# Kernel optimization log

Measured on AMD Instinct MI355X. Metric: run time of the kernel, lower is better.

## Reference

```python
import jax, jax.numpy as jnp
import numpy as np

D_MODEL = 1024
N_HEADS = 16
HEAD_DIM = D_MODEL // N_HEADS
B, S = 4, 2048
NEG = -1000000000.0


def setup_inputs() -> dict:
    key = jax.random.key(0)
    ks = jax.random.split(key, 13)
    sc = 1.0 / np.sqrt(D_MODEL)
    return {
        "query": jax.random.normal(ks[0], (B, S, D_MODEL), jnp.float32),
        "key": jax.random.normal(ks[1], (B, S, D_MODEL), jnp.float32),
        "value": jax.random.normal(ks[2], (B, S, D_MODEL), jnp.float32),
        "mask": jax.random.randint(ks[3], (B, 1, 1, S), 0, 2, jnp.int32),
        "Wq": jax.random.normal(ks[4], (D_MODEL, D_MODEL), jnp.float32) * sc,
        "bq": jax.random.normal(ks[5], (D_MODEL,), jnp.float32) * sc,
        "Wk": jax.random.normal(ks[6], (D_MODEL, D_MODEL), jnp.float32) * sc,
        "bk": jax.random.normal(ks[7], (D_MODEL,), jnp.float32) * sc,
        "Wv": jax.random.normal(ks[8], (D_MODEL, D_MODEL), jnp.float32) * sc,
        "bv": jax.random.normal(ks[9], (D_MODEL,), jnp.float32) * sc,
        "Wo": jax.random.normal(ks[10], (D_MODEL, D_MODEL), jnp.float32) * sc,
        "bo": jax.random.normal(ks[11], (D_MODEL,), jnp.float32) * sc,
    }


def _split_heads(x):
    b, s, _ = x.shape
    return x.reshape(b, s, N_HEADS, HEAD_DIM).transpose(0, 2, 1, 3)  # (B,H,S,Dh)


def reference(query, key, value, mask, Wq, bq, Wk, bk, Wv, bv, Wo, bo):
    # torch Linear: y = x @ W.T + b
    Q = _split_heads(query @ Wq.T + bq)
    K = _split_heads(key @ Wk.T + bk)
    V = _split_heads(value @ Wv.T + bv)
    scores = jnp.einsum("bhqd,bhkd->bhqk", Q, K) / np.sqrt(HEAD_DIM)
    scores = jnp.where(mask == 0, NEG, scores)
    probs = jax.nn.softmax(scores, axis=-1)
    ctx = jnp.einsum("bhqk,bhkd->bhqd", probs, V)
    ctx = ctx.transpose(0, 2, 1, 3).reshape(query.shape[0], query.shape[1], D_MODEL)
    return ctx @ Wo.T + bo
```

## Files before the change

kernel.cpp:

```cpp
#include <hip/hip_runtime.h>


typedef __bf16 bf16x8 __attribute__((ext_vector_type(8)));
typedef __bf16 bf16x4 __attribute__((ext_vector_type(4)));
typedef float  f32x4  __attribute__((ext_vector_type(4)));

#define LOG2E 1.44269504088896340736f
#define SCALE_Q (0.125f * LOG2E)
#define MBIAS_L2 (-1.44269504e9f)

__device__ inline unsigned short f2bf(float f) {
  unsigned int u = __float_as_uint(f);
  u = u + 0x7FFF + ((u >> 16) & 1);
  return (unsigned short)(u >> 16);
}
__device__ inline void gload16(const void* g, void* l) {
  __builtin_amdgcn_global_load_lds(
      (const __attribute__((address_space(1))) void*)g,
      (__attribute__((address_space(3))) void*)l, 16, 0, 0);
}
__device__ inline bf16x8 cvt8(const float* p) {
  float4 a = *(const float4*)p, b = *(const float4*)(p + 4);
  bf16x8 v;
  v[0] = (__bf16)a.x; v[1] = (__bf16)a.y; v[2] = (__bf16)a.z; v[3] = (__bf16)a.w;
  v[4] = (__bf16)b.x; v[5] = (__bf16)b.y; v[6] = (__bf16)b.z; v[7] = (__bf16)b.w;
  return v;
}

struct CvtJob { const float* s; unsigned short* d; int n8; };
struct CvtJobs { CvtJob j[7]; };
__global__ void cvt_all(CvtJobs J) {
  CvtJob jb = J.j[blockIdx.y];
  int i = blockIdx.x * 256 + threadIdx.x;
  if (i < jb.n8) *(bf16x8*)(jb.d + (size_t)i * 8) = cvt8(jb.s + (size_t)i * 8);
}

struct ProjJob { const unsigned short* A; const unsigned short* W;
                 const float* bias; unsigned short* out; float scale; };
struct ProjJobs { ProjJob j[3]; };

__global__ __launch_bounds__(256, 2) void gemm_qkv(ProjJobs J) {
  __shared__ __align__(16) unsigned short Al[128 * 32];
  __shared__ __align__(16) unsigned short Wl[128 * 32];
  const int z = blockIdx.z;
  const ProjJob jb = J.j[z];
  const int tid = threadIdx.x, lane = tid & 63, w = tid >> 6;
  const int lid = lane & 15, lg = lane >> 4;
  const int c0 = blockIdx.x * 128, t0 = blockIdx.y * 128;
  const int wm = (w & 1) * 64, wn = (w >> 1) * 64;
  const unsigned short* Ml = (z == 2) ? Al : Wl;
  const unsigned short* Nl = (z == 2) ? Wl : Al;

  f32x4 acc[4][4];
#pragma unroll
  for (int i = 0; i < 4; i++)
#pragma unroll
    for (int j = 0; j < 4; j++) acc[i][j] = (f32x4){0.f, 0.f, 0.f, 0.f};

  for (int kt = 0; kt < 1024; kt += 32) {
    __syncthreads();
#pragma unroll
    for (int i = 0; i < 2; i++) {
      int c = i * 256 + tid, r = c >> 2, ko = (c & 3) * 8;
      gload16(jb.A + (size_t)(t0 + r) * 1024 + kt + ko, &Al[c * 8]);
      gload16(jb.W + (size_t)(c0 + r) * 1024 + kt + ko, &Wl[c * 8]);
    }
    __syncthreads();
    bf16x8 mf[4], nf[4];
#pragma unroll
    for (int mi = 0; mi < 4; mi++)
      mf[mi] = *(const bf16x8*)(&Ml[(wm + mi * 16 + lid) * 32 + lg * 8]);
#pragma unroll
    for (int ni = 0; ni < 4; ni++)
      nf[ni] = *(const bf16x8*)(&Nl[(wn + ni * 16 + lid) * 32 + lg * 8]);
#pragma unroll
    for (int mi = 0; mi < 4; mi++)
#pragma unroll
      for (int ni = 0; ni < 4; ni++)
        acc[mi][ni] = __builtin_amdgcn_mfma_f32_16x16x32_bf16(mf[mi], nf[ni],
                                                              acc[mi][ni], 0, 0, 0);
  }

  if (z < 2) {
    const float scale = jb.scale;
#pragma unroll
    for (int mi = 0; mi < 4; mi++) {
      int colb = c0 + wm + mi * 16 + lg * 4;
      float4 b4 = *(const float4*)(&jb.bias[colb]);
#pragma unroll
      for (int ni = 0; ni < 4; ni++) {
        int token = t0 + wn + ni * 16 + lid;
        ushort4 st;
        st.x = f2bf((acc[mi][ni][0] + b4.x) * scale);
        st.y = f2bf((acc[mi][ni][1] + b4.y) * scale);
        st.z = f2bf((acc[mi][ni][2] + b4.z) * scale);
        st.w = f2bf((acc[mi][ni][3] + b4.w) * scale);
        *(ushort4*)(&jb.out[(size_t)token * 1024 + colb]) = st;
      }
    }
  } else {
    const int b = t0 >> 11;
#pragma unroll
    for (int ni = 0; ni < 4; ni++) {
      int col = c0 + wn + ni * 16 + lid;
      int h = col >> 6, d = col & 63;
      float bv = jb.bias[col];
#pragma unroll
      for (int mi = 0; mi < 4; mi++) {
        int s = (t0 & 2047) + wm + mi * 16 + lg * 4;
        ushort4 st;
        st.x = f2bf(acc[mi][ni][0] + bv);
        st.y = f2bf(acc[mi][ni][1] + bv);
        st.z = f2bf(acc[mi][ni][2] + bv);
        st.w = f2bf(acc[mi][ni][3] + bv);
        *(ushort4*)(&jb.out[(size_t)((b * 16 + h) * 64 + d) * 2048 + s]) = st;
      }
    }
  }
}

__global__ __launch_bounds__(256, 2) void gemm_o(
    const unsigned short* __restrict__ A, const unsigned short* __restrict__ W,
    const float* __restrict__ bias, float* __restrict__ C) {
  __shared__ __align__(16) unsigned short Al[128 * 32];
  __shared__ __align__(16) unsigned short Wl[128 * 32];
  const int tid = threadIdx.x, lane = tid & 63, w = tid >> 6;
  const int lid = lane & 15, lg = lane >> 4;
  const int c0 = blockIdx.x * 128, t0 = blockIdx.y * 128;
  const int wc = (w & 1) * 64, wt = (w >> 1) * 64;
  f32x4 acc[4][4];
#pragma unroll
  for (int i = 0; i < 4; i++)
#pragma unroll
    for (int j = 0; j < 4; j++) acc[i][j] = (f32x4){0.f, 0.f, 0.f, 0.f};

  for (int kt = 0; kt < 1024; kt += 32) {
    __syncthreads();
#pragma unroll
    for (int i = 0; i < 2; i++) {
      int c = i * 256 + tid, r = c >> 2, ko = (c & 3) * 8;
      gload16(A + (size_t)(t0 + r) * 1024 + kt + ko, &Al[c * 8]);
      gload16(W + (size_t)(c0 + r) * 1024 + kt + ko, &Wl[c * 8]);
    }
    __syncthreads();
    bf16x8 aw[4], bt[4];
#pragma unroll
    for (int mi = 0; mi < 4; mi++)
      aw[mi] = *(const bf16x8*)(&Wl[(wc + mi * 16 + lid) * 32 + lg * 8]);
#pragma unroll
    for (int ni = 0; ni < 4; ni++)
      bt[ni] = *(const bf16x8*)(&Al[(wt + ni * 16 + lid) * 32 + lg * 8]);
#pragma unroll
    for (int mi = 0; mi < 4; mi++)
#pragma unroll
      for (int ni = 0; ni < 4; ni++)
        acc[mi][ni] = __builtin_amdgcn_mfma_f32_16x16x32_bf16(aw[mi], bt[ni],
                                                              acc[mi][ni], 0, 0, 0);
  }
#pragma unroll
  for (int mi = 0; mi < 4; mi++) {
    int colb = c0 + wc + mi * 16 + lg * 4;
    float4 b4 = *(const float4*)(&bias[colb]);
#pragma unroll
    for (int ni = 0; ni < 4; ni++) {
      int token = t0 + wt + ni * 16 + lid;
      float4 st;
      st.x = acc[mi][ni][0] + b4.x;
      st.y = acc[mi][ni][1] + b4.y;
      st.z = acc[mi][ni][2] + b4.z;
      st.w = acc[mi][ni][3] + b4.w;
      *(float4*)(&C[(size_t)token * 1024 + colb]) = st;
    }
  }
}

__global__ __launch_bounds__(256, 2) void attn(
    const unsigned short* __restrict__ Qp,
    const unsigned short* __restrict__ Kp,
    const unsigned short* __restrict__ Vt,
    const int* __restrict__ maskp,
    unsigned short* __restrict__ ctx) {
  __shared__ __align__(16) unsigned short Klds[128 * 64];
  __shared__ __align__(16) unsigned short Vlds[64 * 128];
  __shared__ __align__(16) float mbias[128];

  const int tid = threadIdx.x, lane = tid & 63, w = tid >> 6;
  const int lid = lane & 15, lg = lane >> 4;
  const int q0 = blockIdx.x * 128, bh = blockIdx.y;
  const int b = bh >> 4, h = bh & 15;
  const int wq = w * 32;
  const int x7 = lid & 7;

  bf16x8 qf[2][2];
#pragma unroll
  for (int nt = 0; nt < 2; nt++)
#pragma unroll
    for (int ks = 0; ks < 2; ks++) {
      int qrow = b * 2048 + q0 + wq + nt * 16 + lid;
      qf[nt][ks] = *(const bf16x8*)(Qp + (size_t)qrow * 1024 + h * 64 + ks * 32 + lg * 8);
    }

  f32x4 Ot[4][2];
#pragma unroll
  for (int dt = 0; dt < 4; dt++)
#pragma unroll
    for (int qt = 0; qt < 2; qt++) Ot[dt][qt] = (f32x4){0.f, 0.f, 0.f, 0.f};
  float lrow[2] = {0.f, 0.f};

  const unsigned short* Kg = Kp + (size_t)(b * 2048) * 1024 + h * 64;
  const unsigned short* Vg = Vt + (size_t)bh * 64 * 2048;
  const int* mg = maskp + b * 2048;

  for (int kt = 0; kt < 16; kt++) {
    const int k0 = kt * 128;
    __syncthreads();
#pragma unroll
    for (int i = 0; i < 4; i++) {
      int c = i * 256 + tid, r = c >> 3, gsw = (c & 7) ^ (r & 7);
      gload16(Kg + (size_t)(k0 + r) * 1024 + gsw * 8, &Klds[c * 8]);
    }
#pragma unroll
    for (int i = 0; i < 4; i++) {
      int c = i * 256 + tid, d = c >> 4, gsw = (c & 15) ^ (d & 7);
      gload16(Vg + (size_t)d * 2048 + k0 + gsw * 8, &Vlds[c * 8]);
    }
    if (tid < 128) mbias[tid] = (mg[k0 + tid] == 0) ? MBIAS_L2 : 0.0f;
    __syncthreads();

#pragma unroll
    for (int hf = 0; hf < 2; hf++) {
      f32x4 accS[4][2];
#pragma unroll
      for (int mt = 0; mt < 4; mt++) {
        const f32x4 mb4 = *(const f32x4*)(&mbias[hf * 64 + mt * 16 + lg * 4]);
        accS[mt][0] = mb4;
        accS[mt][1] = mb4;
      }
#pragma unroll
      for (int ks = 0; ks < 2; ks++) {
        int koff = ((ks * 4 + lg) ^ x7) * 8;
#pragma unroll
        for (int mt = 0; mt < 4; mt++) {
          bf16x8 a = *(const bf16x8*)(&Klds[(hf * 64 + mt * 16 + lid) * 64 + koff]);
          accS[mt][0] = __builtin_amdgcn_mfma_f32_16x16x32_bf16(a, qf[0][ks], accS[mt][0], 0, 0, 0);
          accS[mt][1] = __builtin_amdgcn_mfma_f32_16x16x32_bf16(a, qf[1][ks], accS[mt][1], 0, 0, 0);
        }
      }

      bf16x8 pb[2][2];
#pragma unroll
      for (int nt = 0; nt < 2; nt++) {
        f32x4 ps = (f32x4){0.f, 0.f, 0.f, 0.f};
#pragma unroll
        for (int mt = 0; mt < 4; mt++) {
          int half = (mt & 1) * 4;
#pragma unroll
          for (int r = 0; r < 4; r++) {
            float p = __builtin_amdgcn_exp2f(accS[mt][nt][r]);
            ps[r] += p;
            pb[mt >> 1][nt][half + r] = (__bf16)p;
          }
        }
        float lsum = (ps[0] + ps[1]) + (ps[2] + ps[3]);
        lsum += __shfl_xor(lsum, 16);
        lsum += __shfl_xor(lsum, 32);
        lrow[nt] += lsum;
      }

#pragma unroll
      for (int c = 0; c < 2; c++) {
        int cg = hf * 2 + c;
        int glo = ((4 * cg + (lg >> 1)) ^ x7) * 8 + (lg & 1) * 4;
        int ghi = ((4 * cg + 2 + (lg >> 1)) ^ x7) * 8 + (lg & 1) * 4;
#pragma unroll
        for (int dt = 0; dt < 4; dt++) {
          const unsigned short* vrow = &Vlds[(dt * 16 + lid) * 128];
          bf16x4 lo = *(const bf16x4*)(&vrow[glo]);
          bf16x4 hi = *(const bf16x4*)(&vrow[ghi]);
          bf16x8 av = __builtin_shufflevector(lo, hi, 0, 1, 2, 3, 4, 5, 6, 7);
#pragma unroll
          for (int qt = 0; qt < 2; qt++)
            Ot[dt][qt] = __builtin_amdgcn_mfma_f32_16x16x32_bf16(av, pb[c][qt], Ot[dt][qt], 0, 0, 0);
        }
      }
    }
  }

#pragma unroll
  for (int qt = 0; qt < 2; qt++) {
    float inv = 1.0f / lrow[qt];
    int qrow = b * 2048 + q0 + wq + qt * 16 + lid;
#pragma unroll
    for (int dt = 0; dt < 4; dt++) {
      ushort4 st;
      st.x = f2bf(Ot[dt][qt][0] * inv);
      st.y = f2bf(Ot[dt][qt][1] * inv);
      st.z = f2bf(Ot[dt][qt][2] * inv);
      st.w = f2bf(Ot[dt][qt][3] * inv);
      *(ushort4*)(&ctx[(size_t)qrow * 1024 + h * 64 + dt * 16 + lg * 4]) = st;
    }
  }
}

extern "C" void kernel_launch(void* const* d_in, const int* in_sizes, int n_in,
                              void* d_out, int out_size, void* d_ws, size_t ws_size,
                              hipStream_t stream) {
  const float* q  = (const float*)d_in[0];
  const float* k  = (const float*)d_in[1];
  const float* v  = (const float*)d_in[2];
  const int*   mk = (const int*)d_in[3];
  const float* Wq = (const float*)d_in[4];
  const float* bq = (const float*)d_in[5];
  const float* Wk = (const float*)d_in[6];
  const float* bk = (const float*)d_in[7];
  const float* Wv = (const float*)d_in[8];
  const float* bv = (const float*)d_in[9];
  const float* Wo = (const float*)d_in[10];
  const float* bo = (const float*)d_in[11];

  const size_t NTOK = (size_t)8192 * 1024;
  const size_t NW = (size_t)1024 * 1024;

  unsigned short* qb  = (unsigned short*)d_ws;
  unsigned short* kb  = qb + NTOK;
  unsigned short* vb  = kb + NTOK;
  unsigned short* Qp  = vb + NTOK;
  unsigned short* Kp  = Qp + NTOK;
  unsigned short* Vt  = Kp + NTOK;
  unsigned short* Wqb = Vt + NTOK;
  unsigned short* Wkb = Wqb + NW;
  unsigned short* Wvb = Wkb + NW;
  unsigned short* Wob = Wvb + NW;
  unsigned short* ctx = qb;

  CvtJobs J;
  J.j[0] = {q, qb, (int)(NTOK / 8)};
  J.j[1] = {k, kb, (int)(NTOK / 8)};
  J.j[2] = {v, vb, (int)(NTOK / 8)};
  J.j[3] = {Wq, Wqb, (int)(NW / 8)};
  J.j[4] = {Wk, Wkb, (int)(NW / 8)};
  J.j[5] = {Wv, Wvb, (int)(NW / 8)};
  J.j[6] = {Wo, Wob, (int)(NW / 8)};
  cvt_all<<<dim3(4096, 7), 256, 0, stream>>>(J);

  ProjJobs P;
  P.j[0] = {qb, Wqb, bq, Qp, SCALE_Q};
  P.j[1] = {kb, Wkb, bk, Kp, 1.0f};
  P.j[2] = {vb, Wvb, bv, Vt, 1.0f};
  gemm_qkv<<<dim3(8, 64, 3), 256, 0, stream>>>(P);

  attn<<<dim3(16, 64), 256, 0, stream>>>(Qp, Kp, Vt, mk, ctx);
  gemm_o<<<dim3(8, 64), 256, 0, stream>>>(ctx, Wob, bo, (float*)d_out);
}
```

Baseline: 362.0 us.

## Double-buffer K/V tiles in attention, preload mask, compute row sums via MFMA

The attention kernel now double-buffers the K and V LDS tiles, issuing the async global-to-LDS loads for the next key tile before computing on the current one, with a single barrier per iteration. The whole mask row is converted to a bias array in LDS once up front. Row sums of the probabilities are computed with an MFMA against a ones vector instead of scalar adds and cross-lane shuffles, and s_setprio is raised around the MFMA sections. LDS use per block goes up substantially (two K/V buffers plus an 8 KB mask array), which may limit occupancy under the launch bounds of 2 blocks per CU.

```diff
diff --git a/kernel.cpp b/kernel.cpp
--- a/kernel.cpp
+++ b/kernel.cpp
@@ -180,9 +180,9 @@
     const unsigned short* __restrict__ Vt,
     const int* __restrict__ maskp,
     unsigned short* __restrict__ ctx) {
-  __shared__ __align__(16) unsigned short Klds[128 * 64];
-  __shared__ __align__(16) unsigned short Vlds[64 * 128];
-  __shared__ __align__(16) float mbias[128];
+  __shared__ __align__(16) unsigned short Klds[2][128 * 64];
+  __shared__ __align__(16) unsigned short Vlds[2][64 * 128];
+  __shared__ __align__(16) float mball[2048];
 
   const int tid = threadIdx.x, lane = tid & 63, w = tid >> 6;
   const int lid = lane & 15, lg = lane >> 4;
@@ -191,6 +191,16 @@
   const int wq = w * 32;
   const int x7 = lid & 7;
 
+  const unsigned short* Kg = Kp + (size_t)(b * 2048) * 1024 + h * 64;
+  const unsigned short* Vg = Vt + (size_t)bh * 64 * 2048;
+  const int* mg = maskp + b * 2048;
+
+#pragma unroll
+  for (int i = 0; i < 8; i++) {
+    int idx = i * 256 + tid;
+    mball[idx] = (mg[idx] == 0) ? MBIAS_L2 : 0.0f;
+  }
+
   bf16x8 qf[2][2];
 #pragma unroll
   for (int nt = 0; nt < 2; nt++)
@@ -205,67 +215,77 @@
   for (int dt = 0; dt < 4; dt++)
 #pragma unroll
     for (int qt = 0; qt < 2; qt++) Ot[dt][qt] = (f32x4){0.f, 0.f, 0.f, 0.f};
-  float lrow[2] = {0.f, 0.f};
-
-  const unsigned short* Kg = Kp + (size_t)(b * 2048) * 1024 + h * 64;
-  const unsigned short* Vg = Vt + (size_t)bh * 64 * 2048;
-  const int* mg = maskp + b * 2048;
-
-  for (int kt = 0; kt < 16; kt++) {
-    const int k0 = kt * 128;
-    __syncthreads();
+  f32x4 acc_l[2] = {(f32x4){0.f, 0.f, 0.f, 0.f}, (f32x4){0.f, 0.f, 0.f, 0.f}};
+  bf16x8 ones8;
+#pragma unroll
+  for (int i = 0; i < 8; i++) ones8[i] = (__bf16)1.0f;
+
+  auto stage_kv = [&](unsigned short* Kl, unsigned short* Vl, int k0) {
 #pragma unroll
     for (int i = 0; i < 4; i++) {
       int c = i * 256 + tid, r = c >> 3, gsw = (c & 7) ^ (r & 7);
-      gload16(Kg + (size_t)(k0 + r) * 1024 + gsw * 8, &Klds[c * 8]);
+      gload16(Kg + (size_t)(k0 + r) * 1024 + gsw * 8, Kl + c * 8);
     }
 #pragma unroll
     for (int i = 0; i < 4; i++) {
       int c = i * 256 + tid, d = c >> 4, gsw = (c & 15) ^ (d & 7);
-      gload16(Vg + (size_t)d * 2048 + k0 + gsw * 8, &Vlds[c * 8]);
-    }
-    if (tid < 128) mbias[tid] = (mg[k0 + tid] == 0) ? MBIAS_L2 : 0.0f;
-    __syncthreads();
+      gload16(Vg + (size_t)d * 2048 + k0 + gsw * 8, Vl + c * 8);
+    }
+  };
+
+  stage_kv(Klds[0], Vlds[0], 0);
+  __syncthreads();
+
+  int cur = 0;
+  for (int kt = 0; kt < 16; kt++) {
+    if (kt < 15) stage_kv(Klds[cur ^ 1], Vlds[cur ^ 1], (kt + 1) * 128);
+
+    const unsigned short* Kl = Klds[cur];
+    const unsigned short* Vl = Vlds[cur];
+    const float* mb = mball + kt * 128;
 
 #pragma unroll
     for (int hf = 0; hf < 2; hf++) {
       f32x4 accS[4][2];
 #pragma unroll
       for (int mt = 0; mt < 4; mt++) {
-        const f32x4 mb4 = *(const f32x4*)(&mbias[hf * 64 + mt * 16 + lg * 4]);
+        const f32x4 mb4 = *(const f32x4*)(&mb[hf * 64 + mt * 16 + lg * 4]);
         accS[mt][0] = mb4;
         accS[mt][1] = mb4;
       }
+      __builtin_amdgcn_s_setprio(1);
 #pragma unroll
       for (int ks = 0; ks < 2; ks++) {
         int koff = ((ks * 4 + lg) ^ x7) * 8;
 #pragma unroll
         for (int mt = 0; mt < 4; mt++) {
-          bf16x8 a = *(const bf16x8*)(&Klds[(hf * 64 + mt * 16 + lid) * 64 + koff]);
+          bf16x8 a = *(const bf16x8*)(&Kl[(hf * 64 + mt * 16 + lid) * 64 + koff]);
           accS[mt][0] = __builtin_amdgcn_mfma_f32_16x16x32_bf16(a, qf[0][ks], accS[mt][0], 0, 0, 0);
           accS[mt][1] = __builtin_amdgcn_mfma_f32_16x16x32_bf16(a, qf[1][ks], accS[mt][1], 0, 0, 0);
         }
       }
+      __builtin_amdgcn_s_setprio(0);
 
       bf16x8 pb[2][2];
 #pragma unroll
       for (int nt = 0; nt < 2; nt++) {
-        f32x4 ps = (f32x4){0.f, 0.f, 0.f, 0.f};
 #pragma unroll
         for (int mt = 0; mt < 4; mt++) {
           int half = (mt & 1) * 4;
 #pragma unroll
           for (int r = 0; r < 4; r++) {
             float p = __builtin_amdgcn_exp2f(accS[mt][nt][r]);
-            ps[r] += p;
             pb[mt >> 1][nt][half + r] = (__bf16)p;
           }
         }
-        float lsum = (ps[0] + ps[1]) + (ps[2] + ps[3]);
-        lsum += __shfl_xor(lsum, 16);
-        lsum += __shfl_xor(lsum, 32);
-        lrow[nt] += lsum;
-      }
+      }
+
+      __builtin_amdgcn_s_setprio(1);
+#pragma unroll
+      for (int c = 0; c < 2; c++)
+#pragma unroll
+        for (int qt = 0; qt < 2; qt++)
+          acc_l[qt] = __builtin_amdgcn_mfma_f32_16x16x32_bf16(ones8, pb[c][qt], acc_l[qt], 0, 0, 0);
 
 #pragma unroll
       for (int c = 0; c < 2; c++) {
@@ -274,7 +294,7 @@
         int ghi = ((4 * cg + 2 + (lg >> 1)) ^ x7) * 8 + (lg & 1) * 4;
 #pragma unroll
         for (int dt = 0; dt < 4; dt++) {
-          const unsigned short* vrow = &Vlds[(dt * 16 + lid) * 128];
+          const unsigned short* vrow = &Vl[(dt * 16 + lid) * 128];
           bf16x4 lo = *(const bf16x4*)(&vrow[glo]);
           bf16x4 hi = *(const bf16x4*)(&vrow[ghi]);
           bf16x8 av = __builtin_shufflevector(lo, hi, 0, 1, 2, 3, 4, 5, 6, 7);
@@ -283,12 +303,16 @@
             Ot[dt][qt] = __builtin_amdgcn_mfma_f32_16x16x32_bf16(av, pb[c][qt], Ot[dt][qt], 0, 0, 0);
         }
       }
-    }
+      __builtin_amdgcn_s_setprio(0);
+    }
+
+    __syncthreads();
+    cur ^= 1;
   }
 
 #pragma unroll
   for (int qt = 0; qt < 2; qt++) {
-    float inv = 1.0f / lrow[qt];
+    float inv = 1.0f / acc_l[qt][0];
     int qrow = b * 2048 + q0 + wq + qt * 16 + lid;
 #pragma unroll
     for (int dt = 0; dt < 4; dt++) {
```

Result: no change. 357.2 us (-1.3%).
